# Kernel optimization log

Measured on AMD Instinct MI355X. Metric: run time of the kernel, lower is better.

The kernel has to match this reference:

```python
import jax, jax.numpy as jnp
import numpy as np

B, T, D, H = 2, 2048, 1024, 16
DH = D // H

def setup_inputs() -> dict:
    key = jax.random.key(0)
    k1, k2, k3 = jax.random.split(key, 3)
    x = jax.random.normal(k1, (B, T, D), dtype=jnp.float32)
    Wqkv = jax.random.normal(k2, (D, 3 * D), dtype=jnp.float32) * (1.0 / np.sqrt(D))
    Wo = jax.random.normal(k3, (D, D), dtype=jnp.float32) * (1.0 / np.sqrt(D))
    return {"x": x, "Wqkv": Wqkv, "Wo": Wo}

def reference(x, Wqkv, Wo):
    b, t, d = x.shape
    qkv = x @ Wqkv                      # [B,T,3D]
    q, k, v = jnp.split(qkv, 3, axis=-1)
    q = q.reshape(b, t, H, DH)          # [B,T,H,DH]
    k = k.reshape(b, t, H, DH)
    v = v.reshape(b, t, H, DH)
    scale = 1.0 / np.sqrt(DH).astype(np.float32)
    scores = jnp.einsum('bqhd,bkhd->bhqk', q, k) * scale  # [B,H,T,T]
    causal = jnp.tril(jnp.ones((t, t), dtype=bool))       # True = keep
    scores = jnp.where(causal, scores, jnp.finfo(scores.dtype).min)
    attn = jax.nn.softmax(scores, axis=-1)
    y = jnp.einsum('bhqk,bkhd->bqhd', attn, v)            # [B,T,H,DH]
    y = y.reshape(b, t, d)
    return y @ Wo
```

## Files before the change

### kernel.cpp

```cpp
#include <hip/hip_runtime.h>
#include <stdint.h>

typedef __attribute__((ext_vector_type(8))) short short8;
typedef __attribute__((ext_vector_type(8))) __bf16 bf16x8;
typedef __attribute__((ext_vector_type(4))) float f32x4;
typedef __attribute__((ext_vector_type(2))) unsigned int u32x2;

#define T_SEQ 2048

static __device__ __forceinline__ ushort f2bf(float f) {
  uint32_t u = __float_as_uint(f);
  u += 0x7fffu + ((u >> 16) & 1u);
  return (ushort)(u >> 16);
}

static __device__ __forceinline__ uint32_t cvtpk(float lo, float hi) {
  uint32_t r;
  asm("v_cvt_pk_bf16_f32 %0, %1, %2" : "=v"(r) : "v"(lo), "v"(hi));
  return r;
}

static __device__ __forceinline__ f32x4 mfma16(short8 a, short8 b, f32x4 c) {
  return __builtin_amdgcn_mfma_f32_16x16x32_bf16(
      __builtin_bit_cast(bf16x8, a), __builtin_bit_cast(bf16x8, b), c, 0, 0, 0);
}

static __device__ __forceinline__ void gload16(const ushort* g, char* l) {
  __builtin_amdgcn_global_load_lds(
      (const __attribute__((address_space(1))) void*)g,
      (__attribute__((address_space(3))) void*)l, 16, 0, 0);
}

__global__ __launch_bounds__(256) void prep_k(const float* __restrict__ x,
                                              const float* __restrict__ Wqkv,
                                              const float* __restrict__ Wo,
                                              ushort* __restrict__ xb,
                                              ushort* __restrict__ WqkvT,
                                              ushort* __restrict__ WoT) {
  if (blockIdx.x < 2048) {
    int i = (blockIdx.x * 256 + threadIdx.x) * 8;
    float4 a = *(const float4*)(x + i);
    float4 b = *(const float4*)(x + i + 4);
    short8 o;
    ((ushort*)&o)[0] = f2bf(a.x); ((ushort*)&o)[1] = f2bf(a.y);
    ((ushort*)&o)[2] = f2bf(a.z); ((ushort*)&o)[3] = f2bf(a.w);
    ((ushort*)&o)[4] = f2bf(b.x); ((ushort*)&o)[5] = f2bf(b.y);
    ((ushort*)&o)[6] = f2bf(b.z); ((ushort*)&o)[7] = f2bf(b.w);
    *(short8*)(xb + i) = o;
    return;
  }
  __shared__ ushort t[64][65];
  int tb = blockIdx.x - 2048;
  const float* in;
  ushort* out;
  int N, byl;
  if (tb < 768) { in = Wqkv; out = WqkvT; N = 3072; byl = tb >> 4; }
  else          { in = Wo;   out = WoT;   N = 1024; byl = (tb - 768) >> 4; }
  const int K = 1024;
  const int bk = (tb & 15) * 64, bn = byl * 64;
  const int r = threadIdx.x >> 2, c0 = (threadIdx.x & 3) << 4;
  const float* src = in + (size_t)(bk + r) * N + bn + c0;
#pragma unroll
  for (int q = 0; q < 4; ++q) {
    float4 a = *(const float4*)(src + q * 4);
    t[r][c0 + q * 4 + 0] = f2bf(a.x);
    t[r][c0 + q * 4 + 1] = f2bf(a.y);
    t[r][c0 + q * 4 + 2] = f2bf(a.z);
    t[r][c0 + q * 4 + 3] = f2bf(a.w);
  }
  __syncthreads();
  short8 o0, o1;
#pragma unroll
  for (int j = 0; j < 8; ++j) {
    ((ushort*)&o0)[j] = t[c0 + j][r];
    ((ushort*)&o1)[j] = t[c0 + 8 + j][r];
  }
  ushort* dst = out + (size_t)(bn + r) * K + bk + c0;
  *(short8*)(dst) = o0;
  *(short8*)(dst + 8) = o1;
}

__global__ __launch_bounds__(1024) void gemm192(const ushort* __restrict__ A,
                                                const ushort* __restrict__ Bt,
                                                ushort* __restrict__ C,
                                                int Ndim) {
  __shared__ char sA[2][32768];
  __shared__ char sB[2][24576];
  const int tid = threadIdx.x;
  const int lane = tid & 63, wid = tid >> 6;
  const int wm = wid >> 2, wn = wid & 3;
  const int lc = lane & 15, lg = lane >> 4;
  const int bm = blockIdx.x * 256, bn = blockIdx.y * 192;
  const int lane16 = lane << 4;

  f32x4 acc[4][3] = {};

#define STAGE192(tt, bb)                                                    \
  do {                                                                      \
    _Pragma("unroll") for (int i_ = 0; i_ < 4; ++i_) {                      \
      int c_ = tid + i_ * 1024;                                             \
      if (c_ < 3584) {                                                      \
        if (c_ < 2048) {                                                    \
          int row_ = c_ >> 3;                                               \
          int cbl_ = (c_ & 7) << 4;                                         \
          int ce_ = (cbl_ ^ ((row_ & 7) << 4)) >> 1;                        \
          gload16(A + (size_t)(bm + row_) * 1024 + (tt) * 64 + ce_,         \
                  sA[bb] + ((c_ << 4) - lane16));                           \
        } else {                                                            \
          int c2_ = c_ - 2048;                                              \
          int row_ = c2_ >> 3;                                              \
          int cbl_ = (c2_ & 7) << 4;                                        \
          int ce_ = (cbl_ ^ ((row_ & 7) << 4)) >> 1;                        \
          gload16(Bt + (size_t)(bn + row_) * 1024 + (tt) * 64 + ce_,        \
                  sB[bb] + ((c2_ << 4) - lane16));                          \
        }                                                                   \
      }                                                                     \
    }                                                                       \
  } while (0)

  STAGE192(0, 0);
  STAGE192(1, 1);

  for (int t = 0; t < 16; ++t) {
    const int cur = t & 1;
    if (t < 15) {
      if (wid < 8) asm volatile("s_waitcnt vmcnt(4)" ::: "memory");
      else         asm volatile("s_waitcnt vmcnt(3)" ::: "memory");
    } else {
      asm volatile("s_waitcnt vmcnt(0)" ::: "memory");
    }
    __builtin_amdgcn_s_barrier();
    __builtin_amdgcn_sched_barrier(0);
#pragma unroll
    for (int ks = 0; ks < 2; ++ks) {
      const int kb = ks * 64 + lg * 16;
      short8 af[4], bf[3];
#pragma unroll
      for (int mf = 0; mf < 4; ++mf) {
        int row = wm * 64 + mf * 16 + lc;
        af[mf] = *(const short8*)&sA[cur][(row << 7) + (kb ^ ((row & 7) << 4))];
      }
#pragma unroll
      for (int nf = 0; nf < 3; ++nf) {
        int row = wn * 48 + nf * 16 + lc;
        bf[nf] = *(const short8*)&sB[cur][(row << 7) + (kb ^ ((row & 7) << 4))];
      }
      __builtin_amdgcn_s_setprio(1);
#pragma unroll
      for (int mf = 0; mf < 4; ++mf)
#pragma unroll
        for (int nf = 0; nf < 3; ++nf)
          acc[mf][nf] = mfma16(af[mf], bf[nf], acc[mf][nf]);
      __builtin_amdgcn_s_setprio(0);
    }
    asm volatile("s_waitcnt lgkmcnt(0)" ::: "memory");
    __builtin_amdgcn_sched_barrier(0);
    __builtin_amdgcn_s_barrier();
    __builtin_amdgcn_sched_barrier(0);
    if (t + 2 < 16) STAGE192(t + 2, cur);
  }
#undef STAGE192

#pragma unroll
  for (int mf = 0; mf < 4; ++mf) {
    int rowb = bm + wm * 64 + mf * 16 + lg * 4;
#pragma unroll
    for (int nf = 0; nf < 3; ++nf) {
      int col = bn + wn * 48 + nf * 16 + lc;
#pragma unroll
      for (int r = 0; r < 4; ++r)
        C[(size_t)(rowb + r) * Ndim + col] = f2bf(acc[mf][nf][r]);
    }
  }
}

__global__ __launch_bounds__(1024) void gemm128p(const ushort* __restrict__ A,
                                                 const ushort* __restrict__ Bt,
                                                 void* __restrict__ Cv,
                                                 int Ndim, int Kdim, int f32out) {
  __shared__ char sA[2][16384];
  __shared__ char sB[2][16384];
  const int tid = threadIdx.x;
  const int lane = tid & 63, wid = tid >> 6;
  const int wm = wid >> 2, wn = wid & 3;
  const int lc = lane & 15, lg = lane >> 4;
  const int bm = blockIdx.x * 128, bn = blockIdx.y * 128;
  const int lane16 = lane << 4;
  const int nk = Kdim >> 6;

  f32x4 acc[2][2] = {};

#define STAGE128(tt, bb)                                                   \
  do {                                                                     \
    {                                                                      \
      int c_ = tid;                                  \
      int row_ = c_ >> 3;                                                  \
      int cbl_ = (c_ & 7) << 4;                                            \
      int ce_ = (cbl_ ^ ((row_ & 7) << 4)) >> 1;                           \
      gload16(A + (size_t)(bm + row_) * Kdim + (tt) * 64 + ce_,            \
              sA[bb] + ((c_ << 4) - lane16));                              \
    }                                                                      \
    {                                                                      \
      int c_ = tid;                                  \
      int row_ = c_ >> 3;                                                  \
      int cbl_ = (c_ & 7) << 4;                                            \
      int ce_ = (cbl_ ^ ((row_ & 7) << 4)) >> 1;                           \
      gload16(Bt + (size_t)(bn + row_) * Kdim + (tt) * 64 + ce_,           \
              sB[bb] + ((c_ << 4) - lane16));                              \
    }                                                                      \
  } while (0)

  STAGE128(0, 0);
  STAGE128(1, 1);

  for (int t = 0; t < nk; ++t) {
    const int cur = t & 1;
    if (t < nk - 1) asm volatile("s_waitcnt vmcnt(2)" ::: "memory");
    else            asm volatile("s_waitcnt vmcnt(0)" ::: "memory");
    __builtin_amdgcn_s_barrier();
    __builtin_amdgcn_sched_barrier(0);
#pragma unroll
    for (int ks = 0; ks < 2; ++ks) {
      const int kb = ks * 64 + lg * 16;
      short8 af[2], bfr[2];
#pragma unroll
      for (int m = 0; m < 2; ++m) {
        int row = wm * 32 + m * 16 + lc;
        af[m] = *(const short8*)&sA[cur][(row << 7) + (kb ^ ((row & 7) << 4))];
      }
#pragma unroll
      for (int n = 0; n < 2; ++n) {
        int row = wn * 32 + n * 16 + lc;
        bfr[n] = *(const short8*)&sB[cur][(row << 7) + (kb ^ ((row & 7) << 4))];
      }
      __builtin_amdgcn_s_setprio(1);
#pragma unroll
      for (int m = 0; m < 2; ++m)
#pragma unroll
        for (int n = 0; n < 2; ++n)
          acc[m][n] = mfma16(af[m], bfr[n], acc[m][n]);
      __builtin_amdgcn_s_setprio(0);
    }
    asm volatile("s_waitcnt lgkmcnt(0)" ::: "memory");
    __builtin_amdgcn_sched_barrier(0);
    __builtin_amdgcn_s_barrier();
    __builtin_amdgcn_sched_barrier(0);
    if (t + 2 < nk) STAGE128(t + 2, cur);
  }
#undef STAGE128

#pragma unroll
  for (int m = 0; m < 2; ++m) {
    int rowb = bm + wm * 32 + m * 16 + lg * 4;
#pragma unroll
    for (int n = 0; n < 2; ++n) {
      int col = bn + wn * 32 + n * 16 + lc;
      if (f32out) {
        float* C = (float*)Cv;
#pragma unroll
        for (int r = 0; r < 4; ++r)
          C[(size_t)(rowb + r) * Ndim + col] = acc[m][n][r];
      } else {
        ushort* C = (ushort*)Cv;
#pragma unroll
        for (int r = 0; r < 4; ++r)
          C[(size_t)(rowb + r) * Ndim + col] = f2bf(acc[m][n][r]);
      }
    }
  }
}

__global__ __launch_bounds__(512) void attn_k(const ushort* __restrict__ qkv,
                                              ushort* __restrict__ Y) {
  __shared__ char sK[8192];
  __shared__ char sV[8192];
  __shared__ char sP[16384];
  __shared__ float sL[8][16];
  const int tid = threadIdx.x;
  const int lane = tid & 63, wid = tid >> 6;
  const int lc = lane & 15, lg = lane >> 4;
  const int orig = blockIdx.x;
  const int xcd = orig & 7, slot = orig >> 3;
  int tile, bhl;
  if (slot < 32) { tile = slot >> 2;              bhl = slot & 3; }
  else           { tile = 15 - ((slot - 32) >> 2); bhl = (slot - 32) & 3; }
  const int bh = xcd * 4 + bhl;
  const int b = bh >> 4, h = bh & 15;
  char* sPw = sP + (wid << 11);

  const ushort* base = qkv + (size_t)b * T_SEQ * 3072 + h * 64;
  const int q0 = tile * 128 + wid * 16;

  const int kt = tid >> 3, kce = (tid & 7) << 3, kcb = kce << 1;
  const int ksw = (kt & 7) << 4;
  const int vt = tid & 63, vd0 = (tid >> 6) << 3;
  const ushort* kbase = base + 1024;
  const ushort* vbase = base + 2048;

  short8 qf[2];
#pragma unroll
  for (int ks = 0; ks < 2; ++ks)
    qf[ks] = *(const short8*)(base + (size_t)(q0 + lc) * 3072 + ks * 32 + lg * 8);

  f32x4 o[4] = {};
  float lsum = 0.f;

  const float cexp = 0.125f * 1.4426950408889634f;
  const int nkb = 2 * (tile + 1);
  const int qmaxw = q0 + 15;

  short8 kr = *(const short8*)(kbase + (size_t)kt * 3072 + kce);
  short8 vr = *(const short8*)(vbase + (size_t)vt * 3072 + vd0);

  for (int kb = 0; kb < nkb; ++kb) {
    __syncthreads();
    *(short8*)&sK[(kt << 7) + (kcb ^ ksw)] = kr;
#pragma unroll
    for (int j = 0; j < 8; ++j) {
      int d = vd0 + j;
      *(ushort*)&sV[(d << 7) + ((2 * vt) ^ ((d & 7) << 4))] = ((const ushort*)&vr)[j];
    }
    __syncthreads();
    if (kb + 1 < nkb) {
      kr = *(const short8*)(kbase + (size_t)((kb + 1) * 64 + kt) * 3072 + kce);
      vr = *(const short8*)(vbase + (size_t)((kb + 1) * 64 + vt) * 3072 + vd0);
    }
    if (kb * 64 > qmaxw) continue;

    f32x4 S[4] = {};
    __builtin_amdgcn_s_setprio(1);
#pragma unroll
    for (int ks = 0; ks < 2; ++ks) {
      int kbyt = ks * 64 + lg * 16;
      short8 kf[4];
#pragma unroll
      for (int n = 0; n < 4; ++n) {
        int row = n * 16 + lc;
        kf[n] = *(const short8*)&sK[(row << 7) + (kbyt ^ ((row & 7) << 4))];
      }
#pragma unroll
      for (int n = 0; n < 4; ++n)
        S[n] = mfma16(kf[n], qf[ks], S[n]);
    }
    __builtin_amdgcn_s_setprio(0);

    const bool diag = (kb * 64 + 63 > q0);
    {
      int q = q0 + lc;
      float lacc = 0.f;
#pragma unroll
      for (int n = 0; n < 4; ++n) {
        int kg = kb * 64 + n * 16 + lg * 4;
        f32x4 pe;
#pragma unroll
        for (int r = 0; r < 4; ++r) {
          pe[r] = exp2f(S[n][r] * cexp);
          if (diag && (kg + r > q)) pe[r] = 0.f;
        }
        lacc += (pe[0] + pe[1]) + (pe[2] + pe[3]);
        u32x2 w;
        w[0] = cvtpk(pe[0], pe[1]);
        w[1] = cvtpk(pe[2], pe[3]);
        int colb = n * 32 + lg * 8;
        *(u32x2*)&sPw[(lc << 7) + (colb ^ ((lc & 7) << 4))] = w;
      }
      lsum += lacc;
    }
    asm volatile("" ::: "memory");
    __builtin_amdgcn_s_setprio(1);
#pragma unroll
    for (int ks = 0; ks < 2; ++ks) {
      int kbyt = ks * 64 + lg * 16;
      short8 pf = *(const short8*)&sPw[(lc << 7) + (kbyt ^ ((lc & 7) << 4))];
      short8 vf[4];
#pragma unroll
      for (int dn = 0; dn < 4; ++dn) {
        int row = dn * 16 + lc;
        vf[dn] = *(const short8*)&sV[(row << 7) + (kbyt ^ ((row & 7) << 4))];
      }
#pragma unroll
      for (int dn = 0; dn < 4; ++dn)
        o[dn] = mfma16(pf, vf[dn], o[dn]);
    }
    __builtin_amdgcn_s_setprio(0);
  }
  {
    float v = lsum;
    v += __shfl_xor(v, 16);
    v += __shfl_xor(v, 32);
    sL[wid][lc] = 1.0f / v;
  }
  asm volatile("" ::: "memory");
  {
    float lr[4];
#pragma unroll
    for (int r = 0; r < 4; ++r) lr[r] = sL[wid][lg * 4 + r];
#pragma unroll
    for (int dn = 0; dn < 4; ++dn) {
#pragma unroll
      for (int r = 0; r < 4; ++r) {
        int t = q0 + lg * 4 + r;
        Y[(size_t)(b * T_SEQ + t) * 1024 + h * 64 + dn * 16 + lc] =
            f2bf(o[dn][r] * lr[r]);
      }
    }
  }
}

extern "C" void kernel_launch(void* const* d_in, const int* in_sizes, int n_in,
                              void* d_out, int out_size, void* d_ws, size_t ws_size,
                              hipStream_t stream) {
  const float* x    = (const float*)d_in[0];
  const float* Wqkv = (const float*)d_in[1];
  const float* Wo   = (const float*)d_in[2];
  for (int i = 0; i < n_in; ++i) {
    if (in_sizes[i] == 4194304) x = (const float*)d_in[i];
    else if (in_sizes[i] == 3145728) Wqkv = (const float*)d_in[i];
    else if (in_sizes[i] == 1048576) Wo = (const float*)d_in[i];
  }
  float* out = (float*)d_out;

  ushort* xb    = (ushort*)d_ws;
  ushort* WqkvT = xb + (size_t)4096 * 1024;
  ushort* WoT   = WqkvT + (size_t)3072 * 1024;
  ushort* QKV   = WoT + (size_t)1024 * 1024;
  ushort* Yb    = QKV + (size_t)4096 * 3072;

  prep_k<<<3072, 256, 0, stream>>>(x, Wqkv, Wo, xb, WqkvT, WoT);
  gemm192<<<dim3(16, 16), 1024, 0, stream>>>(xb, WqkvT, QKV, 3072);
  attn_k<<<512, 512, 0, stream>>>(QKV, Yb);
  gemm128p<<<dim3(32, 8), 1024, 0, stream>>>(Yb, WoT, out, 1024, 1024, 1);
}
```

Measured before the change: 106.1 us.

## Pair causal query tiles in one 1024-thread attention block sharing K/V staging

The attention kernel now launches 256 blocks of 1024 threads. Each block holds two complementary query tiles (p and 15-p) for the same head, so every block does the same amount of causal work and K/V tiles staged once in shared memory serve both. The K and V global loads are split between wave halves, with waves 0-7 loading K and waves 8-15 loading V, instead of every thread loading both. This is meant to balance the causal triangle across blocks and halve K/V staging traffic. In exchange it doubles the P scratch buffer, and the larger blocks may limit occupancy and make the barriers more costly.

Result: slower. 108.3 us (+2.0%).

```diff
diff --git a/kernel.cpp b/kernel.cpp
--- a/kernel.cpp
+++ b/kernel.cpp
@@ -193,7 +193,7 @@
 #define STAGE128(tt, bb)                                                   \
   do {                                                                     \
     {                                                                      \
-      int c_ = tid;                                  \
+      int c_ = tid;                                                        \
       int row_ = c_ >> 3;                                                  \
       int cbl_ = (c_ & 7) << 4;                                            \
       int ce_ = (cbl_ ^ ((row_ & 7) << 4)) >> 1;                           \
@@ -201,7 +201,7 @@
               sA[bb] + ((c_ << 4) - lane16));                              \
     }                                                                      \
     {                                                                      \
-      int c_ = tid;                                  \
+      int c_ = tid;                                                        \
       int row_ = c_ >> 3;                                                  \
       int cbl_ = (c_ & 7) << 4;                                            \
       int ce_ = (cbl_ ^ ((row_ & 7) << 4)) >> 1;                           \
@@ -270,30 +270,31 @@
   }
 }
 
-__global__ __launch_bounds__(512) void attn_k(const ushort* __restrict__ qkv,
-                                              ushort* __restrict__ Y) {
+__global__ __launch_bounds__(1024) void attn_k(const ushort* __restrict__ qkv,
+                                               ushort* __restrict__ Y) {
   __shared__ char sK[8192];
   __shared__ char sV[8192];
-  __shared__ char sP[16384];
-  __shared__ float sL[8][16];
+  __shared__ char sP[32768];
+  __shared__ float sL[16][16];
   const int tid = threadIdx.x;
   const int lane = tid & 63, wid = tid >> 6;
   const int lc = lane & 15, lg = lane >> 4;
   const int orig = blockIdx.x;
-  const int xcd = orig & 7, slot = orig >> 3;
-  int tile, bhl;
-  if (slot < 32) { tile = slot >> 2;              bhl = slot & 3; }
-  else           { tile = 15 - ((slot - 32) >> 2); bhl = (slot - 32) & 3; }
+  const int xcd = orig & 7, s = orig >> 3;
+  const int p = s >> 2, bhl = s & 3;
   const int bh = xcd * 4 + bhl;
   const int b = bh >> 4, h = bh & 15;
   char* sPw = sP + (wid << 11);
 
   const ushort* base = qkv + (size_t)b * T_SEQ * 3072 + h * 64;
-  const int q0 = tile * 128 + wid * 16;
-
-  const int kt = tid >> 3, kce = (tid & 7) << 3, kcb = kce << 1;
+  const int tile = (wid < 8) ? p : (15 - p);
+  const int q0 = tile * 128 + (wid & 7) * 16;
+
+  const bool isK = (wid < 8);
+  const int st = tid & 511;
+  const int kt = st >> 3, kce = (st & 7) << 3, kcb = kce << 1;
   const int ksw = (kt & 7) << 4;
-  const int vt = tid & 63, vd0 = (tid >> 6) << 3;
+  const int vt = st & 63, vd0 = (st >> 6) << 3;
   const ushort* kbase = base + 1024;
   const ushort* vbase = base + 2048;
 
@@ -306,24 +307,28 @@
   float lsum = 0.f;
 
   const float cexp = 0.125f * 1.4426950408889634f;
-  const int nkb = 2 * (tile + 1);
+  const int nkb = 32 - 2 * p;
   const int qmaxw = q0 + 15;
 
-  short8 kr = *(const short8*)(kbase + (size_t)kt * 3072 + kce);
-  short8 vr = *(const short8*)(vbase + (size_t)vt * 3072 + vd0);
+  short8 rg;
+  if (isK) rg = *(const short8*)(kbase + (size_t)kt * 3072 + kce);
+  else     rg = *(const short8*)(vbase + (size_t)vt * 3072 + vd0);
 
   for (int kb = 0; kb < nkb; ++kb) {
     __syncthreads();
-    *(short8*)&sK[(kt << 7) + (kcb ^ ksw)] = kr;
-#pragma unroll
-    for (int j = 0; j < 8; ++j) {
-      int d = vd0 + j;
-      *(ushort*)&sV[(d << 7) + ((2 * vt) ^ ((d & 7) << 4))] = ((const ushort*)&vr)[j];
+    if (isK) {
+      *(short8*)&sK[(kt << 7) + (kcb ^ ksw)] = rg;
+    } else {
+#pragma unroll
+      for (int j = 0; j < 8; ++j) {
+        int d = vd0 + j;
+        *(ushort*)&sV[(d << 7) + ((2 * vt) ^ ((d & 7) << 4))] = ((const ushort*)&rg)[j];
+      }
     }
     __syncthreads();
     if (kb + 1 < nkb) {
-      kr = *(const short8*)(kbase + (size_t)((kb + 1) * 64 + kt) * 3072 + kce);
-      vr = *(const short8*)(vbase + (size_t)((kb + 1) * 64 + vt) * 3072 + vd0);
+      if (isK) rg = *(const short8*)(kbase + (size_t)((kb + 1) * 64 + kt) * 3072 + kce);
+      else     rg = *(const short8*)(vbase + (size_t)((kb + 1) * 64 + vt) * 3072 + vd0);
     }
     if (kb * 64 > qmaxw) continue;
 
@@ -428,6 +433,6 @@
 
   prep_k<<<3072, 256, 0, stream>>>(x, Wqkv, Wo, xb, WqkvT, WoT);
   gemm192<<<dim3(16, 16), 1024, 0, stream>>>(xb, WqkvT, QKV, 3072);
-  attn_k<<<512, 512, 0, stream>>>(QKV, Yb);
+  attn_k<<<256, 1024, 0, stream>>>(QKV, Yb);
   gemm128p<<<dim3(32, 8), 1024, 0, stream>>>(Yb, WoT, out, 1024, 1024, 1);
 }
```
